# Kernel tuning notes

Hardware: AMD Instinct MI355X
Metric: run time of the kernel (lower is better)

Reference implementation:

```python
import jax, jax.numpy as jnp
import numpy as np

INPUT_DIM, HID_DIM, OUTPUT_DIM, N = 256, 128, 256, 16384
SCALE = 128 ** (-0.5)


def setup_inputs() -> dict:
    key = jax.random.key(0)
    ks = jax.random.split(key, 11)
    s_in = 1.0 / np.sqrt(INPUT_DIM)
    s_hid = 1.0 / np.sqrt(HID_DIM)
    return {
        "q": jax.random.normal(ks[0], (N, INPUT_DIM), jnp.float32),
        "k": jax.random.normal(ks[1], (N, INPUT_DIM), jnp.float32),
        "v": jax.random.normal(ks[2], (N, INPUT_DIM), jnp.float32),
        "Wq": jax.random.uniform(ks[3], (INPUT_DIM, HID_DIM), jnp.float32, -s_in, s_in),
        "bq": jax.random.uniform(ks[4], (HID_DIM,), jnp.float32, -s_in, s_in),
        "Wk": jax.random.uniform(ks[5], (INPUT_DIM, HID_DIM), jnp.float32, -s_in, s_in),
        "bk": jax.random.uniform(ks[6], (HID_DIM,), jnp.float32, -s_in, s_in),
        "Wv": jax.random.uniform(ks[7], (INPUT_DIM, HID_DIM), jnp.float32, -s_in, s_in),
        "bv": jax.random.uniform(ks[8], (HID_DIM,), jnp.float32, -s_in, s_in),
        "Wo": jax.random.uniform(ks[9], (HID_DIM, OUTPUT_DIM), jnp.float32, -s_hid, s_hid),
        "bo": jax.random.uniform(ks[10], (OUTPUT_DIM,), jnp.float32, -s_hid, s_hid),
    }


def reference(q, k, v, Wq, bq, Wk, bk, Wv, bv, Wo, bo):
    qh = q @ Wq + bq                      # [N, H]
    kh = k @ Wk + bk                      # [N, H]
    vh = v @ Wv + bv                      # [N, H]
    scores = (qh @ kh.T) * SCALE          # [N, N] materialized as in original
    attn = jax.nn.softmax(scores, axis=-1)
    out = attn @ vh                       # [N, H]
    return out @ Wo + bo                  # [N, OUTPUT_DIM]
```

## Files before the change

### kernel.cpp

```cpp
#include <hip/hip_runtime.h>
#include <hip/hip_bf16.h>
#include <stdint.h>


#define N_TOK 16384
#define IN_DIM 256
#define HID 128
#define OUT_DIM 256
#define KVB 32
#define BM 128
#define TOT_TILES (N_TOK / KVB)

typedef __bf16   bf16x8 __attribute__((ext_vector_type(8)));
typedef short    short8 __attribute__((ext_vector_type(8)));
typedef float    f32x4  __attribute__((ext_vector_type(4)));
typedef float    f32x16 __attribute__((ext_vector_type(16)));
typedef uint32_t u32x4  __attribute__((ext_vector_type(4)));

#define MFMA16(a,b,c) __builtin_amdgcn_mfma_f32_16x16x32_bf16((a),(b),(c),0,0,0)
#define MFMA32(a,b,c) __builtin_amdgcn_mfma_f32_32x32x16_bf16((a),(b),(c),0,0,0)
#define EXP2(x) __builtin_amdgcn_exp2f(x)

__device__ __forceinline__ short f2bf(float f) {
    union { float f; uint32_t u; } v; v.f = f;
    uint32_t r = v.u + 0x7FFFu + ((v.u >> 16) & 1u);
    return (short)(r >> 16);
}

__device__ __forceinline__ uint32_t cvtpk(float lo, float hi) {
    uint32_t d;
    asm("v_cvt_pk_bf16_f32 %0, %1, %2" : "=v"(d) : "v"(lo), "v"(hi));
    return d;
}

__device__ __forceinline__ void pswap(uint32_t& a, uint32_t& b) {
    auto r = __builtin_amdgcn_permlane32_swap(a, b, false, false);
    a = r[0]; b = r[1];
}

__device__ __forceinline__ void gl16(const void* g, const void* l) {
    __builtin_amdgcn_global_load_lds(
        (const __attribute__((address_space(1))) void*)g,
        (__attribute__((address_space(3))) void*)l, 16, 0, 0);
}

__global__ void wt4_kernel(const float* __restrict__ Wq, const float* __restrict__ Wk,
                           const float* __restrict__ Wv, const float* __restrict__ Wo,
                           short* __restrict__ tq, short* __restrict__ tk,
                           short* __restrict__ tv, short* __restrict__ to_)
{
    int idx = blockIdx.x * 256 + threadIdx.x;
    int w = idx >> 15, i = idx & 32767;
    if (w < 3) {
        const float* W = (w == 0) ? Wq : (w == 1) ? Wk : Wv;
        short* T = (w == 0) ? tq : (w == 1) ? tk : tv;
        int k = i >> 7, c = i & 127;
        T[c * 256 + k] = f2bf(W[i]);
    } else {
        int k = i >> 8, c = i & 255;
        to_[c * 128 + k] = f2bf(Wo[i]);
    }
}

__global__ __launch_bounds__(256) void proj3_kernel(
    const float* __restrict__ q, const float* __restrict__ k, const float* __restrict__ v,
    const short* __restrict__ tq, const short* __restrict__ tk, const short* __restrict__ tv,
    const float* __restrict__ bq, const float* __restrict__ bk, const float* __restrict__ bv,
    short* __restrict__ qh, short* __restrict__ kh, short* __restrict__ vh,
    float scale_q)
{
    const int y = blockIdx.y;
    const float* X  = (y == 0) ? q  : (y == 1) ? k  : v;
    const short* WT = (y == 0) ? tq : (y == 1) ? tk : tv;
    const float* bias = (y == 0) ? bq : (y == 1) ? bk : bv;
    short* Y = (y == 0) ? qh : (y == 1) ? kh : vh;
    const float post_scale = (y == 0) ? scale_q : 1.0f;

    const int lane = threadIdx.x & 63;
    const int wave = threadIdx.x >> 6;
    const int g = lane >> 4, c = lane & 15;
    const int rowbase = blockIdx.x * 64 + wave * 16;

    bf16x8 a[8];
    const float* xrow = X + (size_t)(rowbase + c) * IN_DIM;
#pragma unroll
    for (int kk = 0; kk < 8; ++kk) {
        const float* p = xrow + kk * 32 + 8 * g;
        float4 f0 = *(const float4*)(p);
        float4 f1 = *(const float4*)(p + 4);
        short8 t;
        t[0]=f2bf(f0.x); t[1]=f2bf(f0.y); t[2]=f2bf(f0.z); t[3]=f2bf(f0.w);
        t[4]=f2bf(f1.x); t[5]=f2bf(f1.y); t[6]=f2bf(f1.z); t[7]=f2bf(f1.w);
        a[kk] = __builtin_bit_cast(bf16x8, t);
    }

    f32x4 acc[8];
#pragma unroll
    for (int nf = 0; nf < 8; ++nf) acc[nf] = (f32x4){0.f, 0.f, 0.f, 0.f};

#pragma unroll
    for (int kk = 0; kk < 8; ++kk) {
#pragma unroll
        for (int nf = 0; nf < 8; ++nf) {
            bf16x8 b = *(const bf16x8*)(WT + (size_t)(c + 16 * nf) * IN_DIM + kk * 32 + 8 * g);
            acc[nf] = MFMA16(a[kk], b, acc[nf]);
        }
    }

#pragma unroll
    for (int nf = 0; nf < 8; ++nf) {
        int col = c + 16 * nf;
        float bval = bias[col];
#pragma unroll
        for (int r = 0; r < 4; ++r) {
            int row = rowbase + 4 * g + r;
            short val = f2bf((acc[nf][r] + bval) * post_scale);
            if (y == 0) {
                Y[(size_t)row * HID + col] = val;
            } else if (y == 1) {
                Y[(size_t)(row >> 5) * 4096 + (col >> 4) * 512 + ((col >> 3) & 1) * 256
                  + (row & 31) * 8 + (col & 7)] = val;
            } else {
                Y[(size_t)(row >> 5) * 4096 + ((row >> 4) & 1) * 2048 + (col >> 5) * 512
                  + ((row >> 3) & 1) * 256 + (col & 31) * 8 + (row & 7)] = val;
            }
        }
    }
}

__global__ __launch_bounds__(256, 3) void flash_kernel(
    const short* __restrict__ qh, const short* __restrict__ kh,
    const short* __restrict__ vh,
    short* __restrict__ Opart, float* __restrict__ Lpart,
    int nsplit)
{
    __shared__ short K_lds[3][KVB * HID];
    __shared__ short V_lds[3][KVB * HID];

    const int tid  = threadIdx.x;
    const int lane = tid & 63;
    const int wave = tid >> 6;
    const int hi   = lane >> 5;
    const int col  = lane & 31;

    const int lid = blockIdx.x;
    const int split = lid >> 7;
    const int qtile = lid & 127;

    const int qb = qtile * BM + wave * 32;
    const int tbase = TOT_TILES / nsplit, trem = TOT_TILES % nsplit;
    const int ntiles = tbase + (split < trem ? 1 : 0);
    const int ktile0 = tbase * split + (split < trem ? split : trem);

    bf16x8 qf[8];
    const short* qrow = qh + (size_t)(qb + col) * HID + 8 * hi;
#pragma unroll
    for (int kk = 0; kk < 8; ++kk)
        qf[kk] = *(const bf16x8*)(qrow + 16 * kk);

    f32x16 o[4];
#pragma unroll
    for (int nf = 0; nf < 4; ++nf)
#pragma unroll
        for (int i = 0; i < 16; ++i) o[nf][i] = 0.f;
    float l_run = 0.f;

    const short* kbase = kh + (size_t)ktile0 * 4096;
    const short* vbase = vh + (size_t)ktile0 * 4096;
    const int lds_off = tid * 8;
    const int frag_off = hi * 256 + col * 8;

    auto stage = [&](int t, int buf) {
        const short* ks = kbase + (size_t)t * 4096 + lds_off;
        const short* vs = vbase + (size_t)t * 4096 + lds_off;
        gl16(ks,        &K_lds[buf][lds_off]);
        gl16(ks + 2048, &K_lds[buf][2048 + lds_off]);
        gl16(vs,        &V_lds[buf][lds_off]);
        gl16(vs + 2048, &V_lds[buf][2048 + lds_off]);
    };

    stage(0, 0);
    if (1 < ntiles) stage(1, 1); else stage(0, 1);
    asm volatile("s_waitcnt vmcnt(4)" ::: "memory");
    __builtin_amdgcn_s_barrier();

    for (int t = 0; t < ntiles; ++t) {
        const int cur = t % 3;
        if (t + 2 < ntiles) stage(t + 2, (t + 2) % 3);
        const short* Kc = &K_lds[cur][0];
        const short* Vc = &V_lds[cur][0];

        f32x16 s0;
#pragma unroll
        for (int i = 0; i < 16; ++i) s0[i] = 0.f;
        __builtin_amdgcn_s_setprio(1);
#pragma unroll
        for (int kk = 0; kk < 8; ++kk) {
            bf16x8 ka = *(const bf16x8*)(Kc + kk * 512 + frag_off);
            s0 = MFMA32(ka, qf[kk], s0);
        }
        __builtin_amdgcn_s_setprio(0);

        bf16x8 pa[2];
        {
            float e[16];
#pragma unroll
            for (int i = 0; i < 16; ++i) e[i] = EXP2(s0[i]);
            l_run += (((e[0]+e[1])+(e[2]+e[3])) + ((e[4]+e[5])+(e[6]+e[7])))
                   + (((e[8]+e[9])+(e[10]+e[11])) + ((e[12]+e[13])+(e[14]+e[15])));
            uint32_t x0 = cvtpk(e[0], e[1]),   x1 = cvtpk(e[2], e[3]);
            uint32_t x2 = cvtpk(e[4], e[5]),   x3 = cvtpk(e[6], e[7]);
            uint32_t x4 = cvtpk(e[8], e[9]),   x5 = cvtpk(e[10], e[11]);
            uint32_t x6 = cvtpk(e[12], e[13]), x7 = cvtpk(e[14], e[15]);
            pswap(x0, x2);  pswap(x1, x3);
            pswap(x4, x6);  pswap(x5, x7);
            u32x4 wA, wB;
            wA[0] = x0; wA[1] = x1; wA[2] = x2; wA[3] = x3;
            wB[0] = x4; wB[1] = x5; wB[2] = x6; wB[3] = x7;
            pa[0] = __builtin_bit_cast(bf16x8, wA);
            pa[1] = __builtin_bit_cast(bf16x8, wB);
        }

        __builtin_amdgcn_s_setprio(1);
#pragma unroll
        for (int ks = 0; ks < 2; ++ks)
#pragma unroll
            for (int nf = 0; nf < 4; ++nf) {
                bf16x8 vf = *(const bf16x8*)(Vc + ks * 2048 + nf * 512
                                             + frag_off);
                o[nf] = MFMA32(pa[ks], vf, o[nf]);
            }
        __builtin_amdgcn_s_setprio(0);

        if (t + 2 < ntiles)      asm volatile("s_waitcnt vmcnt(4)" ::: "memory");
        else if (t + 1 < ntiles) asm volatile("s_waitcnt vmcnt(0)" ::: "memory");
        __builtin_amdgcn_s_barrier();
    }

    {
        uint32_t ax = __builtin_bit_cast(uint32_t, l_run), bx = ax;
        pswap(ax, bx);
        l_run = __builtin_bit_cast(float, ax) + __builtin_bit_cast(float, bx);
    }
    const size_t sbase = (size_t)split * N_TOK + qb;
#pragma unroll
    for (int nf = 0; nf < 4; ++nf)
#pragma unroll
        for (int r = 0; r < 16; ++r) {
            int qr = (r & 3) + 8 * (r >> 2) + 4 * hi;
            Opart[(sbase + qr) * HID + 32 * nf + col] = f2bf(o[nf][r]);
        }
    if (lane < 32)
        Lpart[sbase + col] = l_run;
}

__global__ __launch_bounds__(256) void oproj_kernel(
    const short* __restrict__ Opart, const float* __restrict__ Lpart,
    const short* __restrict__ WoT, const float* __restrict__ bo,
    float* __restrict__ out, int nsplit)
{
    const int lane = threadIdx.x & 63;
    const int wave = threadIdx.x >> 6;
    const int g = lane >> 4, c = lane & 15;
    const int rowbase = blockIdx.x * 64 + wave * 16;
    const int row = rowbase + c;

    float denom = 0.f;
    for (int s = 0; s < nsplit; ++s) denom += Lpart[(size_t)s * N_TOK + row];
    const float inv = 1.0f / denom;

    float osum[4][8];
#pragma unroll
    for (int kk = 0; kk < 4; ++kk)
#pragma unroll
        for (int j = 0; j < 8; ++j) osum[kk][j] = 0.f;
    for (int s = 0; s < nsplit; ++s) {
        const short* orow = Opart + ((size_t)s * N_TOK + row) * HID;
#pragma unroll
        for (int kk = 0; kk < 4; ++kk) {
            bf16x8 vv = *(const bf16x8*)(orow + kk * 32 + 8 * g);
#pragma unroll
            for (int j = 0; j < 8; ++j) osum[kk][j] += (float)vv[j];
        }
    }
    bf16x8 a[4];
#pragma unroll
    for (int kk = 0; kk < 4; ++kk) {
        short8 t;
#pragma unroll
        for (int j = 0; j < 8; ++j) t[j] = f2bf(osum[kk][j] * inv);
        a[kk] = __builtin_bit_cast(bf16x8, t);
    }

    f32x4 acc[16];
#pragma unroll
    for (int nf = 0; nf < 16; ++nf) acc[nf] = (f32x4){0.f, 0.f, 0.f, 0.f};
#pragma unroll
    for (int kk = 0; kk < 4; ++kk)
#pragma unroll
        for (int nf = 0; nf < 16; ++nf) {
            bf16x8 b = *(const bf16x8*)(WoT + (size_t)(c + 16 * nf) * HID + kk * 32 + 8 * g);
            acc[nf] = MFMA16(a[kk], b, acc[nf]);
        }

#pragma unroll
    for (int nf = 0; nf < 16; ++nf) {
        int colo = c + 16 * nf;
        float bval = bo[colo];
#pragma unroll
        for (int r = 0; r < 4; ++r)
            out[(size_t)(rowbase + 4 * g + r) * OUT_DIM + colo] = acc[nf][r] + bval;
    }
}

extern "C" void kernel_launch(void* const* d_in, const int* in_sizes, int n_in,
                              void* d_out, int out_size, void* d_ws, size_t ws_size,
                              hipStream_t stream)
{
    (void)in_sizes; (void)n_in; (void)out_size;
    const float* q  = (const float*)d_in[0];
    const float* k  = (const float*)d_in[1];
    const float* v  = (const float*)d_in[2];
    const float* Wq = (const float*)d_in[3];
    const float* bq = (const float*)d_in[4];
    const float* Wk = (const float*)d_in[5];
    const float* bk = (const float*)d_in[6];
    const float* Wv = (const float*)d_in[7];
    const float* bvp= (const float*)d_in[8];
    const float* Wo = (const float*)d_in[9];
    const float* bo = (const float*)d_in[10];
    float* out = (float*)d_out;

    auto need = [](int ns) -> size_t {
        return (size_t)(4 * 65536)
             + (size_t)3 * N_TOK * HID * 2
             + (size_t)ns * N_TOK * HID * 2
             + (size_t)ns * N_TOK * 4
             + (size_t)64 * 1024;
    };
    int nsplit = 6;
    if (ws_size < need(6)) nsplit = 4;
    if (ws_size < need(4)) nsplit = 2;
    if (ws_size < need(2)) nsplit = 1;

    char* base = (char*)d_ws;
    size_t off = 0;
    auto alloc = [&](size_t bytes) -> void* {
        void* p = base + off;
        off = (off + bytes + 255) & ~(size_t)255;
        return p;
    };
    short* wtq = (short*)alloc(128 * 256 * 2);
    short* wtk = (short*)alloc(128 * 256 * 2);
    short* wtv = (short*)alloc(128 * 256 * 2);
    short* wto = (short*)alloc(256 * 128 * 2);
    short* qh  = (short*)alloc((size_t)N_TOK * HID * 2);
    short* khb = (short*)alloc((size_t)N_TOK * HID * 2);
    short* vhb = (short*)alloc((size_t)N_TOK * HID * 2);
    short* Opart = (short*)alloc((size_t)nsplit * N_TOK * HID * 2);
    float* Lp  = (float*)alloc((size_t)nsplit * N_TOK * 4);

    const float SCALE_L2E = 0.088388347648318447f * 1.4426950408889634f;

    wt4_kernel<<<512, 256, 0, stream>>>(Wq, Wk, Wv, Wo, wtq, wtk, wtv, wto);

    proj3_kernel<<<dim3(N_TOK / 64, 3), 256, 0, stream>>>(
        q, k, v, wtq, wtk, wtv, bq, bk, bvp, qh, khb, vhb, SCALE_L2E);

    flash_kernel<<<dim3(128 * nsplit), 256, 0, stream>>>(
        qh, khb, vhb, Opart, Lp, nsplit);

    oproj_kernel<<<N_TOK / 64, 256, 0, stream>>>(
        Opart, Lp, wto, bo, out, nsplit);
}
```

Baseline: 183.8 us.

## Double KV tile to 64 with double buffering and fewer splits

Raises the KV tile size from 32 to 64 rows and switches the LDS pipeline from triple to double buffering, so the buffers fit the same LDS budget. Each iteration now computes two 32-wide score blocks before one larger PV MFMA pass, which halves the barrier and loop overhead per key. The default split count drops from 6 to 4, leaving less partial-output traffic for the combine step. In exchange, each iteration waits on vmcnt(0) with prefetch only one tile ahead, which exposes more load latency and leaves fewer blocks to fill the GPU.

Measured after the change: 194.0 us. 5.6% more time.

```diff
diff --git a/kernel.cpp b/kernel.cpp
--- a/kernel.cpp
+++ b/kernel.cpp
@@ -7,7 +7,7 @@
 #define IN_DIM 256
 #define HID 128
 #define OUT_DIM 256
-#define KVB 32
+#define KVB 64
 #define BM 128
 #define TOT_TILES (N_TOK / KVB)
 
@@ -134,8 +134,8 @@
     short* __restrict__ Opart, float* __restrict__ Lpart,
     int nsplit)
 {
-    __shared__ short K_lds[3][KVB * HID];
-    __shared__ short V_lds[3][KVB * HID];
+    __shared__ short K_lds[2][KVB * HID];
+    __shared__ short V_lds[2][KVB * HID];
 
     const int tid  = threadIdx.x;
     const int lane = tid & 63;
@@ -165,47 +165,51 @@
         for (int i = 0; i < 16; ++i) o[nf][i] = 0.f;
     float l_run = 0.f;
 
-    const short* kbase = kh + (size_t)ktile0 * 4096;
-    const short* vbase = vh + (size_t)ktile0 * 4096;
+    const short* kbase = kh + (size_t)ktile0 * 8192;
+    const short* vbase = vh + (size_t)ktile0 * 8192;
     const int lds_off = tid * 8;
     const int frag_off = hi * 256 + col * 8;
 
     auto stage = [&](int t, int buf) {
-        const short* ks = kbase + (size_t)t * 4096 + lds_off;
-        const short* vs = vbase + (size_t)t * 4096 + lds_off;
+        const short* ks = kbase + (size_t)t * 8192 + lds_off;
+        const short* vs = vbase + (size_t)t * 8192 + lds_off;
         gl16(ks,        &K_lds[buf][lds_off]);
         gl16(ks + 2048, &K_lds[buf][2048 + lds_off]);
+        gl16(ks + 4096, &K_lds[buf][4096 + lds_off]);
+        gl16(ks + 6144, &K_lds[buf][6144 + lds_off]);
         gl16(vs,        &V_lds[buf][lds_off]);
         gl16(vs + 2048, &V_lds[buf][2048 + lds_off]);
+        gl16(vs + 4096, &V_lds[buf][4096 + lds_off]);
+        gl16(vs + 6144, &V_lds[buf][6144 + lds_off]);
     };
 
     stage(0, 0);
-    if (1 < ntiles) stage(1, 1); else stage(0, 1);
-    asm volatile("s_waitcnt vmcnt(4)" ::: "memory");
+    asm volatile("s_waitcnt vmcnt(0)" ::: "memory");
     __builtin_amdgcn_s_barrier();
 
     for (int t = 0; t < ntiles; ++t) {
-        const int cur = t % 3;
-        if (t + 2 < ntiles) stage(t + 2, (t + 2) % 3);
+        const int cur = t & 1;
+        if (t + 1 < ntiles) stage(t + 1, cur ^ 1);
         const short* Kc = &K_lds[cur][0];
         const short* Vc = &V_lds[cur][0];
 
-        f32x16 s0;
-#pragma unroll
-        for (int i = 0; i < 16; ++i) s0[i] = 0.f;
-        __builtin_amdgcn_s_setprio(1);
-#pragma unroll
-        for (int kk = 0; kk < 8; ++kk) {
-            bf16x8 ka = *(const bf16x8*)(Kc + kk * 512 + frag_off);
-            s0 = MFMA32(ka, qf[kk], s0);
-        }
-        __builtin_amdgcn_s_setprio(0);
-
-        bf16x8 pa[2];
-        {
+        bf16x8 pa[4];
+
+#pragma unroll
+        for (int h = 0; h < 2; ++h) {
+            f32x16 s;
+#pragma unroll
+            for (int i = 0; i < 16; ++i) s[i] = 0.f;
+            __builtin_amdgcn_s_setprio(1);
+#pragma unroll
+            for (int kk = 0; kk < 8; ++kk) {
+                bf16x8 ka = *(const bf16x8*)(Kc + h * 4096 + kk * 512 + frag_off);
+                s = MFMA32(ka, qf[kk], s);
+            }
+            __builtin_amdgcn_s_setprio(0);
             float e[16];
 #pragma unroll
-            for (int i = 0; i < 16; ++i) e[i] = EXP2(s0[i]);
+            for (int i = 0; i < 16; ++i) e[i] = EXP2(s[i]);
             l_run += (((e[0]+e[1])+(e[2]+e[3])) + ((e[4]+e[5])+(e[6]+e[7])))
                    + (((e[8]+e[9])+(e[10]+e[11])) + ((e[12]+e[13])+(e[14]+e[15])));
             uint32_t x0 = cvtpk(e[0], e[1]),   x1 = cvtpk(e[2], e[3]);
@@ -217,23 +221,22 @@
             u32x4 wA, wB;
             wA[0] = x0; wA[1] = x1; wA[2] = x2; wA[3] = x3;
             wB[0] = x4; wB[1] = x5; wB[2] = x6; wB[3] = x7;
-            pa[0] = __builtin_bit_cast(bf16x8, wA);
-            pa[1] = __builtin_bit_cast(bf16x8, wB);
+            pa[2 * h]     = __builtin_bit_cast(bf16x8, wA);
+            pa[2 * h + 1] = __builtin_bit_cast(bf16x8, wB);
         }
 
         __builtin_amdgcn_s_setprio(1);
 #pragma unroll
-        for (int ks = 0; ks < 2; ++ks)
+        for (int ks = 0; ks < 4; ++ks)
 #pragma unroll
             for (int nf = 0; nf < 4; ++nf) {
-                bf16x8 vf = *(const bf16x8*)(Vc + ks * 2048 + nf * 512
-                                             + frag_off);
+                bf16x8 vf = *(const bf16x8*)(Vc + (ks >> 1) * 4096 + (ks & 1) * 2048
+                                             + nf * 512 + frag_off);
                 o[nf] = MFMA32(pa[ks], vf, o[nf]);
             }
         __builtin_amdgcn_s_setprio(0);
 
-        if (t + 2 < ntiles)      asm volatile("s_waitcnt vmcnt(4)" ::: "memory");
-        else if (t + 1 < ntiles) asm volatile("s_waitcnt vmcnt(0)" ::: "memory");
+        asm volatile("s_waitcnt vmcnt(0)" ::: "memory");
         __builtin_amdgcn_s_barrier();
     }
 
@@ -338,8 +341,7 @@
              + (size_t)ns * N_TOK * 4
              + (size_t)64 * 1024;
     };
-    int nsplit = 6;
-    if (ws_size < need(6)) nsplit = 4;
+    int nsplit = 4;
     if (ws_size < need(4)) nsplit = 2;
     if (ws_size < need(2)) nsplit = 1;
 
```

## Switch flash attention Q/K/V and probabilities from bf16 to fp8 MFMA

Applied to the files above, without the earlier changes.

Projections now write Q, K and V as fp8 (e4m3) in new tile layouts, and the flash kernel uses 32x32x16 fp8 MFMAs for both QK^T and PV, with P also packed to fp8. The softmax scale moves from the Q projection into the exp2 argument. Global-to-LDS traffic per tile is halved and MFMA throughput per instruction should rise. The cost is a large loss of precision in Q, K, V and the attention weights, which may break accuracy tolerance.

Result: faster. 164.7 us (-10.4%).

```diff
diff --git a/kernel.cpp b/kernel.cpp
--- a/kernel.cpp
+++ b/kernel.cpp
@@ -15,10 +15,11 @@
 typedef short    short8 __attribute__((ext_vector_type(8)));
 typedef float    f32x4  __attribute__((ext_vector_type(4)));
 typedef float    f32x16 __attribute__((ext_vector_type(16)));
-typedef uint32_t u32x4  __attribute__((ext_vector_type(4)));
+typedef uint32_t u32x2  __attribute__((ext_vector_type(2)));
+typedef long     longx2 __attribute__((ext_vector_type(2)));
 
 #define MFMA16(a,b,c) __builtin_amdgcn_mfma_f32_16x16x32_bf16((a),(b),(c),0,0,0)
-#define MFMA32(a,b,c) __builtin_amdgcn_mfma_f32_32x32x16_bf16((a),(b),(c),0,0,0)
+#define MFMA8(a,b,c)  __builtin_amdgcn_mfma_f32_32x32x16_fp8_fp8((a),(b),(c),0,0,0)
 #define EXP2(x) __builtin_amdgcn_exp2f(x)
 
 __device__ __forceinline__ short f2bf(float f) {
@@ -27,10 +28,13 @@
     return (short)(r >> 16);
 }
 
-__device__ __forceinline__ uint32_t cvtpk(float lo, float hi) {
-    uint32_t d;
-    asm("v_cvt_pk_bf16_f32 %0, %1, %2" : "=v"(d) : "v"(lo), "v"(hi));
-    return d;
+template <bool HI>
+__device__ __forceinline__ uint32_t pk_fp8(float a, float b, uint32_t old) {
+    return (uint32_t)__builtin_amdgcn_cvt_pk_fp8_f32(a, b, (int)old, HI);
+}
+
+__device__ __forceinline__ unsigned char f2fp8(float f) {
+    return (unsigned char)(pk_fp8<false>(f, f, 0u) & 0xFFu);
 }
 
 __device__ __forceinline__ void pswap(uint32_t& a, uint32_t& b) {
@@ -66,15 +70,14 @@
     const float* __restrict__ q, const float* __restrict__ k, const float* __restrict__ v,
     const short* __restrict__ tq, const short* __restrict__ tk, const short* __restrict__ tv,
     const float* __restrict__ bq, const float* __restrict__ bk, const float* __restrict__ bv,
-    short* __restrict__ qh, short* __restrict__ kh, short* __restrict__ vh,
-    float scale_q)
+    unsigned char* __restrict__ qh, unsigned char* __restrict__ kh,
+    unsigned char* __restrict__ vh)
 {
     const int y = blockIdx.y;
     const float* X  = (y == 0) ? q  : (y == 1) ? k  : v;
     const short* WT = (y == 0) ? tq : (y == 1) ? tk : tv;
     const float* bias = (y == 0) ? bq : (y == 1) ? bk : bv;
-    short* Y = (y == 0) ? qh : (y == 1) ? kh : vh;
-    const float post_scale = (y == 0) ? scale_q : 1.0f;
+    unsigned char* Y = (y == 0) ? qh : (y == 1) ? kh : vh;
 
     const int lane = threadIdx.x & 63;
     const int wave = threadIdx.x >> 6;
@@ -114,28 +117,30 @@
 #pragma unroll
         for (int r = 0; r < 4; ++r) {
             int row = rowbase + 4 * g + r;
-            short val = f2bf((acc[nf][r] + bval) * post_scale);
+            unsigned char val = f2fp8(acc[nf][r] + bval);
             if (y == 0) {
                 Y[(size_t)row * HID + col] = val;
             } else if (y == 1) {
-                Y[(size_t)(row >> 5) * 4096 + (col >> 4) * 512 + ((col >> 3) & 1) * 256
-                  + (row & 31) * 8 + (col & 7)] = val;
+                Y[(size_t)(row >> 5) * 4096 + (col >> 5) * 1024 + ((col >> 3) & 1) * 512
+                  + (row & 31) * 16 + ((col >> 4) & 1) * 8 + (col & 7)] = val;
             } else {
-                Y[(size_t)(row >> 5) * 4096 + ((row >> 4) & 1) * 2048 + (col >> 5) * 512
-                  + ((row >> 3) & 1) * 256 + (col & 31) * 8 + (row & 7)] = val;
+                Y[(size_t)(row >> 5) * 4096 + (col >> 5) * 1024 + ((row >> 3) & 1) * 512
+                  + (col & 31) * 16 + ((row >> 4) & 1) * 8 + (row & 7)] = val;
             }
         }
     }
 }
 
 __global__ __launch_bounds__(256, 3) void flash_kernel(
-    const short* __restrict__ qh, const short* __restrict__ kh,
-    const short* __restrict__ vh,
+    const unsigned char* __restrict__ qh, const unsigned char* __restrict__ kh,
+    const unsigned char* __restrict__ vh,
     short* __restrict__ Opart, float* __restrict__ Lpart,
     int nsplit)
 {
-    __shared__ short K_lds[3][KVB * HID];
-    __shared__ short V_lds[3][KVB * HID];
+    __shared__ __align__(16) unsigned char K_lds[3][KVB * HID];
+    __shared__ __align__(16) unsigned char V_lds[3][KVB * HID];
+
+    const float kSc = 0.088388347648318447f * 1.4426950408889634f;
 
     const int tid  = threadIdx.x;
     const int lane = tid & 63;
@@ -152,11 +157,11 @@
     const int ntiles = tbase + (split < trem ? 1 : 0);
     const int ktile0 = tbase * split + (split < trem ? split : trem);
 
-    bf16x8 qf[8];
-    const short* qrow = qh + (size_t)(qb + col) * HID + 8 * hi;
+    long qf[8];
+    const unsigned char* qrow = qh + (size_t)(qb + col) * HID + 8 * hi;
 #pragma unroll
     for (int kk = 0; kk < 8; ++kk)
-        qf[kk] = *(const bf16x8*)(qrow + 16 * kk);
+        qf[kk] = *(const long*)(qrow + 16 * kk);
 
     f32x16 o[4];
 #pragma unroll
@@ -165,74 +170,66 @@
         for (int i = 0; i < 16; ++i) o[nf][i] = 0.f;
     float l_run = 0.f;
 
-    const short* kbase = kh + (size_t)ktile0 * 4096;
-    const short* vbase = vh + (size_t)ktile0 * 4096;
-    const int lds_off = tid * 8;
-    const int frag_off = hi * 256 + col * 8;
+    const unsigned char* kbase = kh + (size_t)ktile0 * 4096;
+    const unsigned char* vbase = vh + (size_t)ktile0 * 4096;
+    const int lds_off = tid * 16;
+    const int frag_off = hi * 512 + col * 16;
 
     auto stage = [&](int t, int buf) {
-        const short* ks = kbase + (size_t)t * 4096 + lds_off;
-        const short* vs = vbase + (size_t)t * 4096 + lds_off;
-        gl16(ks,        &K_lds[buf][lds_off]);
-        gl16(ks + 2048, &K_lds[buf][2048 + lds_off]);
-        gl16(vs,        &V_lds[buf][lds_off]);
-        gl16(vs + 2048, &V_lds[buf][2048 + lds_off]);
+        gl16(kbase + (size_t)t * 4096 + lds_off, &K_lds[buf][lds_off]);
+        gl16(vbase + (size_t)t * 4096 + lds_off, &V_lds[buf][lds_off]);
     };
 
     stage(0, 0);
     if (1 < ntiles) stage(1, 1); else stage(0, 1);
-    asm volatile("s_waitcnt vmcnt(4)" ::: "memory");
+    asm volatile("s_waitcnt vmcnt(2)" ::: "memory");
     __builtin_amdgcn_s_barrier();
 
     for (int t = 0; t < ntiles; ++t) {
         const int cur = t % 3;
         if (t + 2 < ntiles) stage(t + 2, (t + 2) % 3);
-        const short* Kc = &K_lds[cur][0];
-        const short* Vc = &V_lds[cur][0];
+        const unsigned char* Kc = &K_lds[cur][0];
+        const unsigned char* Vc = &V_lds[cur][0];
 
         f32x16 s0;
 #pragma unroll
         for (int i = 0; i < 16; ++i) s0[i] = 0.f;
         __builtin_amdgcn_s_setprio(1);
 #pragma unroll
-        for (int kk = 0; kk < 8; ++kk) {
-            bf16x8 ka = *(const bf16x8*)(Kc + kk * 512 + frag_off);
-            s0 = MFMA32(ka, qf[kk], s0);
+        for (int p = 0; p < 4; ++p) {
+            longx2 kp = *(const longx2*)(Kc + p * 1024 + frag_off);
+            s0 = MFMA8(kp[0], qf[2 * p],     s0);
+            s0 = MFMA8(kp[1], qf[2 * p + 1], s0);
         }
         __builtin_amdgcn_s_setprio(0);
 
-        bf16x8 pa[2];
+        long pa0, pa1;
         {
             float e[16];
 #pragma unroll
-            for (int i = 0; i < 16; ++i) e[i] = EXP2(s0[i]);
+            for (int i = 0; i < 16; ++i) e[i] = EXP2(s0[i] * kSc);
             l_run += (((e[0]+e[1])+(e[2]+e[3])) + ((e[4]+e[5])+(e[6]+e[7])))
                    + (((e[8]+e[9])+(e[10]+e[11])) + ((e[12]+e[13])+(e[14]+e[15])));
-            uint32_t x0 = cvtpk(e[0], e[1]),   x1 = cvtpk(e[2], e[3]);
-            uint32_t x2 = cvtpk(e[4], e[5]),   x3 = cvtpk(e[6], e[7]);
-            uint32_t x4 = cvtpk(e[8], e[9]),   x5 = cvtpk(e[10], e[11]);
-            uint32_t x6 = cvtpk(e[12], e[13]), x7 = cvtpk(e[14], e[15]);
-            pswap(x0, x2);  pswap(x1, x3);
-            pswap(x4, x6);  pswap(x5, x7);
-            u32x4 wA, wB;
-            wA[0] = x0; wA[1] = x1; wA[2] = x2; wA[3] = x3;
-            wB[0] = x4; wB[1] = x5; wB[2] = x6; wB[3] = x7;
-            pa[0] = __builtin_bit_cast(bf16x8, wA);
-            pa[1] = __builtin_bit_cast(bf16x8, wB);
+            uint32_t A0 = pk_fp8<true>(e[2],  e[3],  pk_fp8<false>(e[0],  e[1],  0u));
+            uint32_t B0 = pk_fp8<true>(e[6],  e[7],  pk_fp8<false>(e[4],  e[5],  0u));
+            uint32_t A1 = pk_fp8<true>(e[10], e[11], pk_fp8<false>(e[8],  e[9],  0u));
+            uint32_t B1 = pk_fp8<true>(e[14], e[15], pk_fp8<false>(e[12], e[13], 0u));
+            pswap(A0, B0);
+            pswap(A1, B1);
+            pa0 = __builtin_bit_cast(long, (u32x2){A0, B0});
+            pa1 = __builtin_bit_cast(long, (u32x2){A1, B1});
         }
 
         __builtin_amdgcn_s_setprio(1);
 #pragma unroll
-        for (int ks = 0; ks < 2; ++ks)
-#pragma unroll
-            for (int nf = 0; nf < 4; ++nf) {
-                bf16x8 vf = *(const bf16x8*)(Vc + ks * 2048 + nf * 512
-                                             + frag_off);
-                o[nf] = MFMA32(pa[ks], vf, o[nf]);
-            }
+        for (int nf = 0; nf < 4; ++nf) {
+            longx2 vp = *(const longx2*)(Vc + nf * 1024 + frag_off);
+            o[nf] = MFMA8(pa0, vp[0], o[nf]);
+            o[nf] = MFMA8(pa1, vp[1], o[nf]);
+        }
         __builtin_amdgcn_s_setprio(0);
 
-        if (t + 2 < ntiles)      asm volatile("s_waitcnt vmcnt(4)" ::: "memory");
+        if (t + 2 < ntiles)      asm volatile("s_waitcnt vmcnt(2)" ::: "memory");
         else if (t + 1 < ntiles) asm volatile("s_waitcnt vmcnt(0)" ::: "memory");
         __builtin_amdgcn_s_barrier();
     }
@@ -333,7 +330,7 @@
 
     auto need = [](int ns) -> size_t {
         return (size_t)(4 * 65536)
-             + (size_t)3 * N_TOK * HID * 2
+             + (size_t)3 * N_TOK * HID
              + (size_t)ns * N_TOK * HID * 2
              + (size_t)ns * N_TOK * 4
              + (size_t)64 * 1024;
@@ -354,18 +351,16 @@
     short* wtk = (short*)alloc(128 * 256 * 2);
     short* wtv = (short*)alloc(128 * 256 * 2);
     short* wto = (short*)alloc(256 * 128 * 2);
-    short* qh  = (short*)alloc((size_t)N_TOK * HID * 2);
-    short* khb = (short*)alloc((size_t)N_TOK * HID * 2);
-    short* vhb = (short*)alloc((size_t)N_TOK * HID * 2);
+    unsigned char* qh  = (unsigned char*)alloc((size_t)N_TOK * HID);
+    unsigned char* khb = (unsigned char*)alloc((size_t)N_TOK * HID);
+    unsigned char* vhb = (unsigned char*)alloc((size_t)N_TOK * HID);
     short* Opart = (short*)alloc((size_t)nsplit * N_TOK * HID * 2);
     float* Lp  = (float*)alloc((size_t)nsplit * N_TOK * 4);
 
-    const float SCALE_L2E = 0.088388347648318447f * 1.4426950408889634f;
-
     wt4_kernel<<<512, 256, 0, stream>>>(Wq, Wk, Wv, Wo, wtq, wtk, wtv, wto);
 
     proj3_kernel<<<dim3(N_TOK / 64, 3), 256, 0, stream>>>(
-        q, k, v, wtq, wtk, wtv, bq, bk, bvp, qh, khb, vhb, SCALE_L2E);
+        q, k, v, wtq, wtk, wtv, bq, bk, bvp, qh, khb, vhb);
 
     flash_kernel<<<dim3(128 * nsplit), 256, 0, stream>>>(
         qh, khb, vhb, Opart, Lp, nsplit);
```
